# Optimization experiments

Measured on AMD Instinct MI355X. Metric: run time of the kernel, lower is better.

The kernel has to match this reference:

```python
import jax, jax.numpy as jnp
import numpy as np

EPS = 1e-5
GN_GROUPS = 4  # ConvBlock groupnorm num_groups

def _conv3d(x, w, b):
    # x: [B,C,D,H,W], w: [O,I,3,3,3]
    y = jax.lax.conv_general_dilated(x, w, (1, 1, 1), 'SAME',
                                     dimension_numbers=('NCDHW', 'OIDHW', 'NCDHW'))
    return y + b[None, :, None, None, None]

def _groupnorm(x, gamma, beta):
    b, c, d, h, w = x.shape
    xg = x.reshape(b, GN_GROUPS, c // GN_GROUPS, d, h, w)
    m = xg.mean(axis=(2, 3, 4, 5), keepdims=True)
    v = xg.var(axis=(2, 3, 4, 5), keepdims=True)
    xn = ((xg - m) * jax.lax.rsqrt(v + EPS)).reshape(b, c, d, h, w)
    return xn * gamma[None, :, None, None, None] + beta[None, :, None, None, None]

def setup_inputs() -> dict:
    key = jax.random.key(0)
    ks = jax.random.split(key, 8)
    B, C, D, H, W = 4, 64, 16, 16, 16
    R = 4
    f = lambda k, s: jax.random.normal(k, s, dtype=jnp.float32) * 0.05
    return {
        'x': jax.random.normal(ks[0], (B, C, D, H, W), dtype=jnp.float32),
        'w_i': f(ks[1], (C, C, 3, 3, 3)), 'b_i': jnp.zeros((C,), jnp.float32),
        'gamma_i': jnp.ones((C,), jnp.float32), 'beta_i': jnp.zeros((C,), jnp.float32),
        'w_q': f(ks[2], (C // R, C)), 'b_q': jnp.zeros((C // R,), jnp.float32),
        'w_k': f(ks[3], (C // R, C)), 'b_k': jnp.zeros((C // R,), jnp.float32),
        'w_v': f(ks[4], (C, C)), 'b_v': jnp.zeros((C,), jnp.float32),
        'w_o': f(ks[5], (C, C, 3, 3, 3)), 'b_o': jnp.zeros((C,), jnp.float32),
        'gamma_o': jnp.ones((C,), jnp.float32), 'beta_o': jnp.zeros((C,), jnp.float32),
    }

def reference(x, w_i, b_i, gamma_i, beta_i, w_q, b_q, w_k, b_k, w_v, b_v,
              w_o, b_o, gamma_o, beta_o):
    # i_conv: Conv3d(3x3x3) -> GroupNorm(4) -> ReLU
    x = jax.nn.relu(_groupnorm(_conv3d(x, w_i, b_i), gamma_i, beta_i))
    b, c, d, h, w = x.shape
    n = d * h * w
    xf = x.reshape(b, c, n)
    # spatial attention (groups=1): conv1x1 projections as channel matmuls
    q = jnp.einsum('oc,bcn->bon', w_q, xf) + b_q[None, :, None]   # [b, c/r, n]
    k = jnp.einsum('oc,bcn->bon', w_k, xf) + b_k[None, :, None]   # [b, c/r, n]
    v = jnp.einsum('oc,bcn->bon', w_v, xf) + b_v[None, :, None]   # [b, c,   n]
    A = jax.nn.softmax(jnp.einsum('bqn,bqm->bnm', q, k), axis=-1)  # [b, n, n]
    # ans = bmm(value, A^T): ans[b,c,m] = sum_n v[b,c,n] * A[b,m,n]
    sa = jnp.einsum('bcn,bmn->bcm', v, A).reshape(b, c, d, h, w)
    # channel attention
    Ac = jax.nn.softmax(jnp.einsum('bcn,bdn->bcd', xf, xf), axis=-1)  # [b, c, c]
    ca = jnp.einsum('bcd,bdn->bcn', Ac, xf).reshape(b, c, d, h, w)
    y = x + sa + ca
    # o_conv
    return jax.nn.relu(_groupnorm(_conv3d(y, w_o, b_o), gamma_o, beta_o))
```

## Files before the change

kernel.cpp:

```cpp
#include <hip/hip_runtime.h>

#define OFF_X1  0
#define OFF_SA  1048576
#define OFF_QT  2097152
#define OFF_KT  2359296
#define OFF_VB  2621440
#define OFF_YT  3145728
#define OFF_XB  3670016
#define OFF_AC  4194304
#define OFF_WBI 4210688
#define OFF_WBO 4265984
#define OFF_PT  4321280
#define OFF_PO  4325376
#define OFF_MS  6422528
#define WS_NEED ((size_t)6553600 * 4)

typedef __attribute__((ext_vector_type(8))) short short8v;
typedef __attribute__((ext_vector_type(4))) short short4v;
typedef __attribute__((ext_vector_type(4))) float f32x4;

__device__ __forceinline__ ushort f2bf(float f) {
  union { float f; unsigned u; } v; v.f = f;
  unsigned r = (v.u + 0x7fffu + ((v.u >> 16) & 1u)) >> 16;
  return (ushort)r;
}
__device__ __forceinline__ float bf2f(ushort u) {
  union { unsigned u; float f; } v; v.u = ((unsigned)u) << 16;
  return v.f;
}
__device__ __forceinline__ float max3f(float a, float b, float c) {
  return fmaxf(fmaxf(a, b), c);
}

__device__ __forceinline__ void gld_lds16(const ushort* g, ushort* l) {
  __builtin_amdgcn_global_load_lds(
      (const __attribute__((address_space(1))) unsigned*)(unsigned long long)g,
      (__attribute__((address_space(3))) unsigned*)(unsigned long long)l,
      16, 0, 0);
}

__global__ __launch_bounds__(256) void cvt_k(const float* __restrict__ x, ushort* __restrict__ xb,
    float* __restrict__ pt, const float* __restrict__ wi, const float* __restrict__ wo,
    ushort* __restrict__ wbi, ushort* __restrict__ wbo, float* __restrict__ acr) {
  __shared__ ushort tl[64 * 72];
  int blk = blockIdx.x;
  int t = threadIdx.x;
  if (blk < 256) {
    int b = blk >> 6;
    int n0 = (blk & 63) * 64;
    int ci = t >> 2, q = t & 3;
    const float* src = x + (size_t)(b * 64 + ci) * 4096 + n0 + q * 16;
    #pragma unroll
    for (int i = 0; i < 4; ++i) {
      float4 v = *reinterpret_cast<const float4*>(src + i * 4);
      tl[(q * 16 + i * 4 + 0) * 72 + ci] = f2bf(v.x);
      tl[(q * 16 + i * 4 + 1) * 72 + ci] = f2bf(v.y);
      tl[(q * 16 + i * 4 + 2) * 72 + ci] = f2bf(v.z);
      tl[(q * 16 + i * 4 + 3) * 72 + ci] = f2bf(v.w);
    }
    __syncthreads();
    int n = t >> 2, qq = t & 3;
    ushort* dst = xb + (size_t)(b * 4096 + n0 + n) * 64 + qq * 16;
    *reinterpret_cast<short8v*>(dst) = *reinterpret_cast<const short8v*>(&tl[n * 72 + qq * 16]);
    *reinterpret_cast<short8v*>(dst + 8) = *reinterpret_cast<const short8v*>(&tl[n * 72 + qq * 16 + 8]);
  } else if (blk < 1120) {
    int idx = (blk - 256) * 256 + t;
    const float* w = idx < 110592 ? wi : wo;
    ushort* wb = idx < 110592 ? wbi : wbo;
    int j = idx < 110592 ? idx : idx - 110592;
    int ci = j & 63, tap = (j >> 6) % 27, co = j / (64 * 27);
    wb[j] = f2bf(w[(co * 64 + ci) * 27 + tap]);
  } else {
    int idx = (blk - 1120) * 256 + t;
    acr[idx] = 0.f;
    if (blk == 1120 && t < 128) pt[t] = 0.f;
  }
}

__global__ __launch_bounds__(256) void conv_mfma_k(const ushort* __restrict__ xt,
    const ushort* __restrict__ wb, const float* __restrict__ bias, float* __restrict__ out,
    float* __restrict__ ptg, const ushort* __restrict__ zbuf) {
  __shared__ __align__(16) ushort xls[2624 * 8];
  __shared__ float sh_st[16];
  int blk = blockIdx.x;
  int h0 = (blk & 3) * 4;
  int d0 = (blk >> 2) & 15;
  int b  = blk >> 6;
  int tid = threadIdx.x;

  const ushort* xtb = xt + (size_t)b * 4096 * 64;
  {
    int wv0 = tid >> 6, ln = tid & 63;
    #pragma unroll
    for (int it = 0; it < 11; ++it) {
      int clbase = (it * 4 + wv0) * 64;
      if (it == 10) {
        if (wv0 != 0) break;
        clbase = 2560;
      }
      int cl = clbase + ln;
      int c2 = cl & 7;
      int rw = cl >> 3;
      int w_s = rw % 18;
      int rowi = rw / 18;
      int dz = rowi / 6, h_s = rowi - dz * 6;
      int d = d0 + dz - 1, h = h0 + h_s - 1, w = w_s - 1;
      int csrc = c2 ^ (w_s & 7);
      const ushort* g = (d >= 0 && d < 16 && h >= 0 && h < 16 && w >= 0 && w < 16)
          ? xtb + (size_t)(d * 256 + h * 16 + w) * 64 + (csrc << 3)
          : zbuf;
      gld_lds16(g, xls + clbase * 8);
    }
  }
  __syncthreads();

  int wv = tid >> 6, l = tid & 63;
  int wn = wv >> 1, wc = wv & 1;
  int lm = l & 15, lg = l >> 4;

  f32x4 acc[2][2] = {};
  const ushort* wbase0 = wb + (size_t)((wc * 2 + 0) * 16 + lm) * 1728 + lg * 8;
  const ushort* wbase1 = wb + (size_t)((wc * 2 + 1) * 16 + lm) * 1728 + lg * 8;

  #pragma unroll 6
  for (int s = 0; s < 54; ++s) {
    int tap = s >> 1, c0h = s & 1;
    int dz = tap / 9, dyx = tap - dz * 9;
    int dy = dyx / 3, dx = dyx - dy * 3;
    int wrow = lm + dx;
    int chunk = ((c0h * 4 + lg) ^ (wrow & 7)) << 3;
    int r0 = ((dz * 6 + wn * 2 + dy) * 18 + wrow) * 64 + chunk;
    short8v a0 = *reinterpret_cast<const short8v*>(&xls[r0]);
    short8v a1 = *reinterpret_cast<const short8v*>(&xls[r0 + 18 * 64]);
    short8v b0 = *reinterpret_cast<const short8v*>(wbase0 + s * 32);
    short8v b1 = *reinterpret_cast<const short8v*>(wbase1 + s * 32);
    acc[0][0] = __builtin_amdgcn_mfma_f32_16x16x32_bf16(a0, b0, acc[0][0], 0, 0, 0);
    acc[0][1] = __builtin_amdgcn_mfma_f32_16x16x32_bf16(a0, b1, acc[0][1], 0, 0, 0);
    acc[1][0] = __builtin_amdgcn_mfma_f32_16x16x32_bf16(a1, b0, acc[1][0], 0, 0, 0);
    acc[1][1] = __builtin_amdgcn_mfma_f32_16x16x32_bf16(a1, b1, acc[1][1], 0, 0, 0);
  }

  float gs[2], gss[2];
  #pragma unroll
  for (int j = 0; j < 2; ++j) {
    gs[j] = 0.f; gss[j] = 0.f;
    int co = (wc * 2 + j) * 16 + lm;
    float bs = bias[co];
    #pragma unroll
    for (int i = 0; i < 2; ++i) {
      int hh = h0 + wn * 2 + i;
      float4 o;
      o.x = acc[i][j][0] + bs; o.y = acc[i][j][1] + bs;
      o.z = acc[i][j][2] + bs; o.w = acc[i][j][3] + bs;
      gs[j]  += o.x + o.y + o.z + o.w;
      gss[j] = fmaf(o.x, o.x, gss[j]); gss[j] = fmaf(o.y, o.y, gss[j]);
      gss[j] = fmaf(o.z, o.z, gss[j]); gss[j] = fmaf(o.w, o.w, gss[j]);
      *reinterpret_cast<float4*>(&out[(size_t)(b * 64 + co) * 4096 + d0 * 256 + hh * 16 + lg * 4]) = o;
    }
  }
  #pragma unroll
  for (int j = 0; j < 2; ++j) {
    #pragma unroll
    for (int off = 32; off > 0; off >>= 1) {
      gs[j]  += __shfl_xor(gs[j], off);
      gss[j] += __shfl_xor(gss[j], off);
    }
    if (l == 0) { sh_st[wv * 4 + j * 2] = gs[j]; sh_st[wv * 4 + j * 2 + 1] = gss[j]; }
  }
  __syncthreads();
  if (tid < 8) {
    int g = tid >> 1, w2 = tid & 1;
    int wcg = g >> 1, j = g & 1;
    float v = sh_st[wcg * 4 + j * 2 + w2] + sh_st[(wcg + 2) * 4 + j * 2 + w2];
    atomicAdd(&ptg[(b * 4 + g) * 2 + w2], v);
  }
}

__global__ __launch_bounds__(256) void gn_apply_k(const float* __restrict__ t, const float* __restrict__ pt,
    const float* __restrict__ gamma, const float* __restrict__ beta, float* __restrict__ out) {
  int idx4 = blockIdx.x * 256 + threadIdx.x;
  int c = (idx4 >> 10) & 63, b = idx4 >> 16;
  int bg = b * 4 + (c >> 4);
  float s0 = pt[bg * 2], ss0 = pt[bg * 2 + 1];
  float m = s0 * (1.f / 65536.f);
  float r = rsqrtf(ss0 * (1.f / 65536.f) - m * m + 1e-5f);
  float ga = r * gamma[c], bb2 = beta[c] - m * r * gamma[c];
  float4 v = *reinterpret_cast<const float4*>(t + (size_t)idx4 * 4);
  float4 o;
  o.x = fmaxf(fmaf(v.x, ga, bb2), 0.f);
  o.y = fmaxf(fmaf(v.y, ga, bb2), 0.f);
  o.z = fmaxf(fmaf(v.z, ga, bb2), 0.f);
  o.w = fmaxf(fmaf(v.w, ga, bb2), 0.f);
  *reinterpret_cast<float4*>(out + (size_t)idx4 * 4) = o;
}

__global__ __launch_bounds__(256) void projgram_k(const float* __restrict__ t0, const float* __restrict__ pt0,
    const float* __restrict__ gamma, const float* __restrict__ beta,
    const float* __restrict__ wq, const float* __restrict__ bq,
    const float* __restrict__ wk, const float* __restrict__ bk,
    const float* __restrict__ wv_, const float* __restrict__ bv,
    ushort* __restrict__ qt, ushort* __restrict__ kt, ushort* __restrict__ vt,
    float* __restrict__ acr) {
  __shared__ __align__(16) float smem[64 * 68];
  int blk = blockIdx.x;
  int tid = threadIdx.x;
  if (blk < 256) {
    float* xls = smem;
    int b = blk >> 6, n0 = (blk & 63) * 64;
    {
      int ci = tid >> 2, q = tid & 3;
      int bg = b * 4 + (ci >> 4);
      float s0 = pt0[bg * 2], ss0 = pt0[bg * 2 + 1];
      float m = s0 * (1.f / 65536.f);
      float rv = rsqrtf(ss0 * (1.f / 65536.f) - m * m + 1e-5f);
      float ga = rv * gamma[ci], bb2 = beta[ci] - m * rv * gamma[ci];
      const float* src = t0 + (size_t)(b * 64 + ci) * 4096 + n0 + q * 16;
      #pragma unroll
      for (int i = 0; i < 4; ++i) {
        float4 v = *reinterpret_cast<const float4*>(src + i * 4);
        float* d = &xls[ci * 68 + q * 16 + i * 4];
        d[0] = fmaxf(fmaf(v.x, ga, bb2), 0.f);
        d[1] = fmaxf(fmaf(v.y, ga, bb2), 0.f);
        d[2] = fmaxf(fmaf(v.z, ga, bb2), 0.f);
        d[3] = fmaxf(fmaf(v.w, ga, bb2), 0.f);
      }
    }
    __syncthreads();
    int n = tid & 63, og = tid >> 6;
    float xr[64];
    #pragma unroll
    for (int c = 0; c < 64; ++c) xr[c] = xls[c * 68 + n];
    if (og < 2) {
      const float* w  = og == 0 ? wq : wk;
      const float* bb = og == 0 ? bq : bk;
      float scale = og == 0 ? 1.4426950408889634f : 1.0f;
      ushort* outp = og == 0 ? qt : kt;
      union { ushort u[16]; short8v v[2]; } pk;
      #pragma unroll
      for (int o = 0; o < 16; ++o) {
        const float* wr = w + o * 64;
        float acc = bb[o];
        #pragma unroll
        for (int c = 0; c < 64; ++c) acc = fmaf(wr[c], xr[c], acc);
        pk.u[o] = f2bf(acc * scale);
      }
      ushort* dst = outp + (size_t)(b * 4096 + n0 + n) * 32;
      *reinterpret_cast<short8v*>(dst) = pk.v[0];
      *reinterpret_cast<short8v*>(dst + 8) = pk.v[1];
      short8v z = {};
      *reinterpret_cast<short8v*>(dst + 16) = z;
      *reinterpret_cast<short8v*>(dst + 24) = z;
    } else {
      int o0 = (og - 2) * 32;
      #pragma unroll
      for (int o = 0; o < 32; ++o) {
        const float* wr = wv_ + (o0 + o) * 64;
        float acc = bv[o0 + o];
        #pragma unroll
        for (int c = 0; c < 64; ++c) acc = fmaf(wr[c], xr[c], acc);
        vt[(size_t)(b * 64 + o0 + o) * 4096 + n0 + n] = f2bf(acc);
      }
    }
  } else {
    ushort* hi = (ushort*)smem;
    ushort* lo = hi + 4096;
    int gblk = blk - 256;
    int b = gblk >> 5, ks = gblk & 31;
    int wv = tid >> 6, l = tid & 63, lm = l & 15, lg = l >> 4;
    int wr = wv >> 1, wd = wv & 1;
    f32x4 acc[2][2] = {};
    int sr = tid >> 2, sq = tid & 3;
    int bg = b * 4 + (sr >> 4);
    float s0p = pt0[bg * 2], ss0p = pt0[bg * 2 + 1];
    float mq = s0p * (1.f / 65536.f);
    float rq = rsqrtf(ss0p * (1.f / 65536.f) - mq * mq + 1e-5f);
    float ga = rq * gamma[sr], bb2 = beta[sr] - mq * rq * gamma[sr];
    const float* xb = t0 + (size_t)b * 262144;

    for (int kt2 = 0; kt2 < 2; ++kt2) {
      int n0 = ks * 128 + kt2 * 64;
      __syncthreads();
      const float* src = xb + (size_t)sr * 4096 + n0 + sq * 16;
      #pragma unroll
      for (int c2 = 0; c2 < 2; ++c2) {
        int chunk = sq * 2 + c2;
        int dchunk = chunk ^ (sr & 7);
        short8v hvv, lvv;
        #pragma unroll
        for (int j = 0; j < 8; ++j) {
          float v = fmaxf(fmaf(src[c2 * 8 + j], ga, bb2), 0.f);
          ushort hb = f2bf(v);
          union { float f; unsigned u; } uu; uu.u = ((unsigned)hb) << 16;
          hvv[j] = (short)hb;
          lvv[j] = (short)f2bf(v - uu.f);
        }
        *reinterpret_cast<short8v*>(hi + sr * 64 + dchunk * 8) = hvv;
        *reinterpret_cast<short8v*>(lo + sr * 64 + dchunk * 8) = lvv;
      }
      __syncthreads();
      #pragma unroll
      for (int kk = 0; kk < 2; ++kk) {
        short8v ah[2], al[2], bh[2], bl[2];
        #pragma unroll
        for (int i = 0; i < 2; ++i) {
          int rc = wr * 32 + i * 16 + lm;
          int ca = ((kk * 4 + lg) ^ (rc & 7)) * 8;
          ah[i] = *reinterpret_cast<const short8v*>(hi + rc * 64 + ca);
          al[i] = *reinterpret_cast<const short8v*>(lo + rc * 64 + ca);
          int rd = wd * 32 + i * 16 + lm;
          int cb = ((kk * 4 + lg) ^ (rd & 7)) * 8;
          bh[i] = *reinterpret_cast<const short8v*>(hi + rd * 64 + cb);
          bl[i] = *reinterpret_cast<const short8v*>(lo + rd * 64 + cb);
        }
        #pragma unroll
        for (int i = 0; i < 2; ++i)
          #pragma unroll
          for (int j = 0; j < 2; ++j) {
            acc[i][j] = __builtin_amdgcn_mfma_f32_16x16x32_bf16(ah[i], bh[j], acc[i][j], 0, 0, 0);
            acc[i][j] = __builtin_amdgcn_mfma_f32_16x16x32_bf16(ah[i], bl[j], acc[i][j], 0, 0, 0);
            acc[i][j] = __builtin_amdgcn_mfma_f32_16x16x32_bf16(al[i], bh[j], acc[i][j], 0, 0, 0);
          }
      }
    }
    float* acb = acr + (size_t)b * 4096;
    #pragma unroll
    for (int i = 0; i < 2; ++i)
      #pragma unroll
      for (int j = 0; j < 2; ++j)
        #pragma unroll
        for (int r = 0; r < 4; ++r) {
          int c = wr * 32 + i * 16 + lg * 4 + r;
          int d = wd * 32 + j * 16 + lm;
          atomicAdd(&acb[c * 64 + d], acc[i][j][r]);
        }
  }
}

#define KP 40
#define VP 72
template<bool SPLIT>
__global__ __launch_bounds__(256) void flash_mfma_k(const ushort* __restrict__ qt,
    const ushort* __restrict__ kt, const ushort* __restrict__ vb, float* __restrict__ sa,
    ushort* __restrict__ pacc, float* __restrict__ pms) {
  __shared__ __align__(16) ushort kls[2][64 * KP];
  __shared__ __align__(16) ushort vls[2][64 * VP];
  __shared__ __align__(16) ushort pls[64 * VP];
  int s, mt, b;
  if (SPLIT) { s = blockIdx.x & 3; mt = (blockIdx.x >> 2) & 63; b = blockIdx.x >> 8; }
  else       { s = 0; mt = blockIdx.x & 63; b = blockIdx.x >> 6; }
  const int NT = SPLIT ? 16 : 64;
  int m0 = mt * 64;
  int kofs = s * 1024;
  int tid = threadIdx.x;
  int w = tid >> 6, l = tid & 63;
  int lm = l & 15, lg = l >> 4;

  short8v qf = *reinterpret_cast<const short8v*>(
      qt + (size_t)(b * 4096 + m0 + w * 16 + lm) * 32 + lg * 8);

  f32x4 acc[4] = {};
  float M = -1e30f, S = 0.f;

  int sr = tid >> 2, sq = tid & 3;
  const ushort* ksrc = kt + (size_t)b * 4096 * 32 + (size_t)kofs * 32 + (size_t)sr * 32 + sq * 8;
  const ushort* vsrc = vb + (size_t)b * 64 * 4096 + (size_t)sr * 4096 + kofs + sq * 16;
  int koff = sr * KP + sq * 8;
  int voff = sr * VP + sq * 16;

  {
    short8v kr = *reinterpret_cast<const short8v*>(ksrc);
    short8v v0 = *reinterpret_cast<const short8v*>(vsrc);
    short8v v1 = *reinterpret_cast<const short8v*>(vsrc + 8);
    *reinterpret_cast<short8v*>(&kls[0][koff]) = kr;
    *reinterpret_cast<short8v*>(&vls[0][voff]) = v0;
    *reinterpret_cast<short8v*>(&vls[0][voff + 8]) = v1;
  }

  ushort* plb = &pls[(w * 16 + lm) * VP];

  #pragma unroll 2
  for (int it = 0; it < NT; ++it) {
    int cur = it & 1;
    int nx = it < NT - 1 ? it + 1 : NT - 1;
    short8v knr = *reinterpret_cast<const short8v*>(ksrc + (size_t)nx * 2048);
    short8v vn0 = *reinterpret_cast<const short8v*>(vsrc + nx * 64);
    short8v vn1 = *reinterpret_cast<const short8v*>(vsrc + nx * 64 + 8);

    __syncthreads();

    const ushort* kb  = &kls[cur][0];
    const ushort* vbk = &vls[cur][0];

    f32x4 sf[4];
    #pragma unroll
    for (int nt = 0; nt < 4; ++nt) {
      short8v kf = *reinterpret_cast<const short8v*>(&kb[(nt * 16 + lm) * KP + lg * 8]);
      f32x4 z = {};
      sf[nt] = __builtin_amdgcn_mfma_f32_16x16x32_bf16(kf, qf, z, 0, 0, 0);
    }

    float t0_ = max3f(sf[0][0], sf[0][1], sf[0][2]);
    float t1_ = max3f(sf[0][3], sf[1][0], sf[1][1]);
    float t2_ = max3f(sf[1][2], sf[1][3], sf[2][0]);
    float t3_ = max3f(sf[2][1], sf[2][2], sf[2][3]);
    float t4_ = max3f(sf[3][0], sf[3][1], sf[3][2]);
    float tmax = fmaxf(max3f(t0_, t1_, t2_), max3f(t3_, t4_, sf[3][3]));
    tmax = fmaxf(tmax, __shfl_xor(tmax, 16));
    tmax = fmaxf(tmax, __shfl_xor(tmax, 32));
    if (!__all(tmax <= M)) {
      float Mn = fmaxf(M, tmax);
      float sc = __builtin_amdgcn_exp2f(M - Mn);
      M = Mn;
      S *= sc;
      #pragma unroll
      for (int ct = 0; ct < 4; ++ct)
        #pragma unroll
        for (int r = 0; r < 4; ++r) acc[ct][r] *= sc;
    }
    float tsum = 0.f;
    float p[16];
    #pragma unroll
    for (int nt = 0; nt < 4; ++nt)
      #pragma unroll
      for (int r = 0; r < 4; ++r) {
        float e = __builtin_amdgcn_exp2f(sf[nt][r] - M);
        p[nt * 4 + r] = e;
        tsum += e;
      }
    tsum += __shfl_xor(tsum, 16);
    tsum += __shfl_xor(tsum, 32);
    S += tsum;

    #pragma unroll
    for (int nt = 0; nt < 4; ++nt) {
      unsigned p01, p23;
      asm("v_cvt_pk_bf16_f32 %0, %1, %2" : "=v"(p01) : "v"(p[nt * 4 + 0]), "v"(p[nt * 4 + 1]));
      asm("v_cvt_pk_bf16_f32 %0, %1, %2" : "=v"(p23) : "v"(p[nt * 4 + 2]), "v"(p[nt * 4 + 3]));
      union { unsigned u[2]; short4v v; } pk;
      pk.u[0] = p01; pk.u[1] = p23;
      *reinterpret_cast<short4v*>(plb + nt * 16 + lg * 4) = pk.v;
    }
    asm volatile("s_waitcnt lgkmcnt(0)" ::: "memory");
    __builtin_amdgcn_sched_barrier(0);

    #pragma unroll
    for (int nh = 0; nh < 2; ++nh) {
      short8v pf = *reinterpret_cast<const short8v*>(plb + nh * 32 + lg * 8);
      #pragma unroll
      for (int ct = 0; ct < 4; ++ct) {
        short8v vf = *reinterpret_cast<const short8v*>(&vbk[(ct * 16 + lm) * VP + nh * 32 + lg * 8]);
        acc[ct] = __builtin_amdgcn_mfma_f32_16x16x32_bf16(vf, pf, acc[ct], 0, 0, 0);
      }
    }

    if (it < NT - 1) {
      *reinterpret_cast<short8v*>(&kls[cur ^ 1][koff]) = knr;
      *reinterpret_cast<short8v*>(&vls[cur ^ 1][voff]) = vn0;
      *reinterpret_cast<short8v*>(&vls[cur ^ 1][voff + 8]) = vn1;
    }
  }

  if (SPLIT) {
    int blk2 = (b * 64 + mt) * 4 + s;
    ushort* pa = pacc + (size_t)blk2 * 4096;
    #pragma unroll
    for (int ct = 0; ct < 4; ++ct)
      #pragma unroll
      for (int r = 0; r < 4; ++r)
        pa[(ct * 16 + lg * 4 + r) * 64 + w * 16 + lm] = f2bf(acc[ct][r]);
    if (l < 16) {
      pms[(size_t)blk2 * 128 + (w * 16 + lm) * 2]     = M;
      pms[(size_t)blk2 * 128 + (w * 16 + lm) * 2 + 1] = S;
    }
  } else {
    float inv = 1.f / S;
    #pragma unroll
    for (int ct = 0; ct < 4; ++ct)
      #pragma unroll
      for (int r = 0; r < 4; ++r)
        sa[(size_t)(b * 64 + ct * 16 + lg * 4 + r) * 4096 + m0 + w * 16 + lm] = acc[ct][r] * inv;
  }
}

template<int NSPLIT>
__global__ __launch_bounds__(256) void ca_apply_k(const float* __restrict__ t0,
    const float* __restrict__ pt0, const float* __restrict__ gamma, const float* __restrict__ beta,
    const float* __restrict__ acr, const float* __restrict__ sa,
    const ushort* __restrict__ pacc, const float* __restrict__ pms, ushort* __restrict__ yt) {
  __shared__ float x1f[64 * 72];
  __shared__ float acf[64 * 72];
  __shared__ float wls[4 * 64];
  int b = blockIdx.x >> 6, mt = blockIdx.x & 63;
  int n0 = mt * 64;
  int tid = threadIdx.x;
  {
    int d = tid >> 2, q = tid & 3;
    int bg = b * 4 + (d >> 4);
    float s0p = pt0[bg * 2], ss0p = pt0[bg * 2 + 1];
    float mq = s0p * (1.f / 65536.f);
    float rq = rsqrtf(ss0p * (1.f / 65536.f) - mq * mq + 1e-5f);
    float ga = rq * gamma[d], bb2 = beta[d] - mq * rq * gamma[d];
    const float* xs = t0 + (size_t)(b * 64 + d) * 4096 + n0 + q * 16;
    const float* as = acr + (size_t)(b * 64 + d) * 64 + q * 16;
    #pragma unroll
    for (int i = 0; i < 4; ++i) {
      float4 v = *reinterpret_cast<const float4*>(xs + i * 4);
      x1f[d * 72 + q * 16 + i * 4 + 0] = fmaxf(fmaf(v.x, ga, bb2), 0.f);
      x1f[d * 72 + q * 16 + i * 4 + 1] = fmaxf(fmaf(v.y, ga, bb2), 0.f);
      x1f[d * 72 + q * 16 + i * 4 + 2] = fmaxf(fmaf(v.z, ga, bb2), 0.f);
      x1f[d * 72 + q * 16 + i * 4 + 3] = fmaxf(fmaf(v.w, ga, bb2), 0.f);
      float4 a = *reinterpret_cast<const float4*>(as + i * 4);
      acf[d * 72 + q * 16 + i * 4 + 0] = a.x;
      acf[d * 72 + q * 16 + i * 4 + 1] = a.y;
      acf[d * 72 + q * 16 + i * 4 + 2] = a.z;
      acf[d * 72 + q * 16 + i * 4 + 3] = a.w;
    }
  }
  if (NSPLIT > 1 && tid < 64) {
    int m = tid;
    size_t msb = (size_t)(b * 64 + mt) * NSPLIT * 128;
    float Ms[NSPLIT], Ss[NSPLIT];
    float Mg = -1e30f;
    #pragma unroll
    for (int s = 0; s < NSPLIT; ++s) {
      Ms[s] = pms[msb + s * 128 + m * 2];
      Ss[s] = pms[msb + s * 128 + m * 2 + 1];
      Mg = fmaxf(Mg, Ms[s]);
    }
    float Stot = 0.f;
    #pragma unroll
    for (int s = 0; s < NSPLIT; ++s) {
      float wv = __builtin_amdgcn_exp2f(Ms[s] - Mg);
      wls[s * 64 + m] = wv;
      Stot += wv * Ss[s];
    }
    float inv = 1.f / Stot;
    #pragma unroll
    for (int s = 0; s < NSPLIT; ++s) wls[s * 64 + m] *= inv;
  }
  __syncthreads();
  {
    int r = tid >> 2, q4 = tid & 3;
    float* row = &acf[r * 72 + q4 * 16];
    float mx = -1e30f;
    #pragma unroll
    for (int i = 0; i < 16; ++i) mx = fmaxf(mx, row[i]);
    mx = fmaxf(mx, __shfl_xor(mx, 1));
    mx = fmaxf(mx, __shfl_xor(mx, 2));
    float e[16];
    float sum = 0.f;
    #pragma unroll
    for (int i = 0; i < 16; ++i) { e[i] = __expf(row[i] - mx); sum += e[i]; }
    sum += __shfl_xor(sum, 1);
    sum += __shfl_xor(sum, 2);
    float inv = 1.f / sum;
    #pragma unroll
    for (int i = 0; i < 16; ++i) row[i] = e[i] * inv;
  }
  __syncthreads();
  int m = tid & 63, cg = tid >> 6;
  float sval[16];
  if (NSPLIT > 1) {
    #pragma unroll
    for (int ci = 0; ci < 16; ++ci) sval[ci] = 0.f;
    const ushort* pb = pacc + (size_t)(b * 64 + mt) * NSPLIT * 4096;
    #pragma unroll
    for (int s = 0; s < NSPLIT; ++s) {
      float wv = wls[s * 64 + m];
      #pragma unroll
      for (int ci = 0; ci < 16; ++ci)
        sval[ci] = fmaf(wv, bf2f(pb[s * 4096 + (cg * 16 + ci) * 64 + m]), sval[ci]);
    }
  } else {
    #pragma unroll
    for (int ci = 0; ci < 16; ++ci)
      sval[ci] = sa[(size_t)(b * 64 + cg * 16 + ci) * 4096 + n0 + m];
  }
  float xcol[64];
  #pragma unroll
  for (int d = 0; d < 64; ++d) xcol[d] = x1f[d * 72 + m];
  union { ushort u[16]; short8v v[2]; } pk;
  #pragma unroll
  for (int ci = 0; ci < 16; ++ci) {
    int c = cg * 16 + ci;
    float o = xcol[c] + sval[ci];
    const float* ar = &acf[c * 72];
    #pragma unroll
    for (int d4 = 0; d4 < 16; ++d4) {
      float4 a4 = *reinterpret_cast<const float4*>(ar + d4 * 4);
      o = fmaf(a4.x, xcol[d4 * 4 + 0], o);
      o = fmaf(a4.y, xcol[d4 * 4 + 1], o);
      o = fmaf(a4.z, xcol[d4 * 4 + 2], o);
      o = fmaf(a4.w, xcol[d4 * 4 + 3], o);
    }
    pk.u[ci] = f2bf(o);
  }
  ushort* dst = yt + (size_t)(b * 4096 + n0 + m) * 64 + cg * 16;
  *reinterpret_cast<short8v*>(dst) = pk.v[0];
  *reinterpret_cast<short8v*>(dst + 8) = pk.v[1];
}

extern "C" void kernel_launch(void* const* d_in, const int* in_sizes, int n_in,
                              void* d_out, int out_size, void* d_ws, size_t ws_size,
                              hipStream_t stream) {
  const float* x       = (const float*)d_in[0];
  const float* w_i     = (const float*)d_in[1];
  const float* b_i     = (const float*)d_in[2];
  const float* gamma_i = (const float*)d_in[3];
  const float* beta_i  = (const float*)d_in[4];
  const float* w_q     = (const float*)d_in[5];
  const float* b_q     = (const float*)d_in[6];
  const float* w_k     = (const float*)d_in[7];
  const float* b_k     = (const float*)d_in[8];
  const float* w_v     = (const float*)d_in[9];
  const float* b_v     = (const float*)d_in[10];
  const float* w_o     = (const float*)d_in[11];
  const float* b_o     = (const float*)d_in[12];
  const float* gamma_o = (const float*)d_in[13];
  const float* beta_o  = (const float*)d_in[14];
  float* ws = (float*)d_ws;
  float* t0 = ws + OFF_X1;
  ushort* qt  = (ushort*)(ws + OFF_QT);
  ushort* kt  = (ushort*)(ws + OFF_KT);
  ushort* vbp = (ushort*)(ws + OFF_VB);
  float* yb = ws + OFF_SA;
  ushort* ytp = (ushort*)(ws + OFF_YT);
  ushort* xbp = (ushort*)(ws + OFF_XB);
  float* acr = ws + OFF_AC;
  ushort* wbi = (ushort*)(ws + OFF_WBI);
  ushort* wbo = (ushort*)(ws + OFF_WBO);
  float* pt0 = ws + OFF_PT;
  float* pt1 = pt0 + 32;
  const ushort* zbuf = (const ushort*)(pt0 + 96);
  ushort* pacc = (ushort*)(ws + OFF_PO);
  float* pms  = ws + OFF_MS;
  float* outp = (float*)d_out;
  bool split = ws_size >= WS_NEED;

  cvt_k<<<1184, 256, 0, stream>>>(x, xbp, pt0, w_i, w_o, wbi, wbo, acr);

  conv_mfma_k<<<256, 256, 0, stream>>>(xbp, wbi, b_i, t0, pt0, zbuf);

  projgram_k<<<384, 256, 0, stream>>>(t0, pt0, gamma_i, beta_i,
                                      w_q, b_q, w_k, b_k, w_v, b_v, qt, kt, vbp, acr);

  if (split)
    flash_mfma_k<true><<<1024, 256, 0, stream>>>(qt, kt, vbp, yb, pacc, pms);
  else
    flash_mfma_k<false><<<256, 256, 0, stream>>>(qt, kt, vbp, yb, pacc, pms);

  if (split)
    ca_apply_k<4><<<256, 256, 0, stream>>>(t0, pt0, gamma_i, beta_i, acr, yb, pacc, pms, ytp);
  else
    ca_apply_k<1><<<256, 256, 0, stream>>>(t0, pt0, gamma_i, beta_i, acr, yb, pacc, pms, ytp);

  conv_mfma_k<<<256, 256, 0, stream>>>(ytp, wbo, b_o, t0, pt1, zbuf);
  gn_apply_k<<<1024, 256, 0, stream>>>(t0, pt1, gamma_o, beta_o, outp);
}
```

Baseline: 116.3 us.

## Double threads per block in conv and channel-attention kernels, reorder projgram blocks

The 3D conv kernel moves from 4 to 8 waves per block, each wave covering one 16-channel output slice with 2 MFMA accumulators instead of 4. The channel-attention apply kernel also moves to 512 threads, with each thread handling 8 channels instead of 16. In projgram, the gram-matrix blocks are now scheduled first, ahead of the projection blocks. The aim is more latency hiding and more waves per CU on a grid of only 256 blocks, at the cost of redundant A-operand LDS reads across waves and per-thread redundant xcol loads.

After: 114.8 us. Within noise of the previous version (-1.3%).

```diff
diff --git a/kernel.cpp b/kernel.cpp
--- a/kernel.cpp
+++ b/kernel.cpp
@@ -77,7 +77,7 @@
   }
 }
 
-__global__ __launch_bounds__(256) void conv_mfma_k(const ushort* __restrict__ xt,
+__global__ __launch_bounds__(512) void conv_mfma_k(const ushort* __restrict__ xt,
     const ushort* __restrict__ wb, const float* __restrict__ bias, float* __restrict__ out,
     float* __restrict__ ptg, const ushort* __restrict__ zbuf) {
   __shared__ __align__(16) ushort xls[2624 * 8];
@@ -92,12 +92,10 @@
   {
     int wv0 = tid >> 6, ln = tid & 63;
     #pragma unroll
-    for (int it = 0; it < 11; ++it) {
-      int clbase = (it * 4 + wv0) * 64;
-      if (it == 10) {
-        if (wv0 != 0) break;
-        clbase = 2560;
-      }
+    for (int it = 0; it < 6; ++it) {
+      int clbase;
+      if (it < 5) clbase = (it * 8 + wv0) * 64;
+      else { if (wv0 != 0) break; clbase = 2560; }
       int cl = clbase + ln;
       int c2 = cl & 7;
       int rw = cl >> 3;
@@ -115,12 +113,11 @@
   __syncthreads();
 
   int wv = tid >> 6, l = tid & 63;
-  int wn = wv >> 1, wc = wv & 1;
+  int wc4 = wv & 3, wn = wv >> 2;
   int lm = l & 15, lg = l >> 4;
 
-  f32x4 acc[2][2] = {};
-  const ushort* wbase0 = wb + (size_t)((wc * 2 + 0) * 16 + lm) * 1728 + lg * 8;
-  const ushort* wbase1 = wb + (size_t)((wc * 2 + 1) * 16 + lm) * 1728 + lg * 8;
+  f32x4 acc[2] = {};
+  const ushort* wbase = wb + (size_t)((wc4 * 16 + lm) * 1728) + lg * 8;
 
   #pragma unroll 6
   for (int s = 0; s < 54; ++s) {
@@ -132,46 +129,35 @@
     int r0 = ((dz * 6 + wn * 2 + dy) * 18 + wrow) * 64 + chunk;
     short8v a0 = *reinterpret_cast<const short8v*>(&xls[r0]);
     short8v a1 = *reinterpret_cast<const short8v*>(&xls[r0 + 18 * 64]);
-    short8v b0 = *reinterpret_cast<const short8v*>(wbase0 + s * 32);
-    short8v b1 = *reinterpret_cast<const short8v*>(wbase1 + s * 32);
-    acc[0][0] = __builtin_amdgcn_mfma_f32_16x16x32_bf16(a0, b0, acc[0][0], 0, 0, 0);
-    acc[0][1] = __builtin_amdgcn_mfma_f32_16x16x32_bf16(a0, b1, acc[0][1], 0, 0, 0);
-    acc[1][0] = __builtin_amdgcn_mfma_f32_16x16x32_bf16(a1, b0, acc[1][0], 0, 0, 0);
-    acc[1][1] = __builtin_amdgcn_mfma_f32_16x16x32_bf16(a1, b1, acc[1][1], 0, 0, 0);
-  }
-
-  float gs[2], gss[2];
+    short8v b0 = *reinterpret_cast<const short8v*>(wbase + s * 32);
+    acc[0] = __builtin_amdgcn_mfma_f32_16x16x32_bf16(a0, b0, acc[0], 0, 0, 0);
+    acc[1] = __builtin_amdgcn_mfma_f32_16x16x32_bf16(a1, b0, acc[1], 0, 0, 0);
+  }
+
+  float gs = 0.f, gss = 0.f;
+  int co = wc4 * 16 + lm;
+  float bs = bias[co];
   #pragma unroll
-  for (int j = 0; j < 2; ++j) {
-    gs[j] = 0.f; gss[j] = 0.f;
-    int co = (wc * 2 + j) * 16 + lm;
-    float bs = bias[co];
-    #pragma unroll
-    for (int i = 0; i < 2; ++i) {
-      int hh = h0 + wn * 2 + i;
-      float4 o;
-      o.x = acc[i][j][0] + bs; o.y = acc[i][j][1] + bs;
-      o.z = acc[i][j][2] + bs; o.w = acc[i][j][3] + bs;
-      gs[j]  += o.x + o.y + o.z + o.w;
-      gss[j] = fmaf(o.x, o.x, gss[j]); gss[j] = fmaf(o.y, o.y, gss[j]);
-      gss[j] = fmaf(o.z, o.z, gss[j]); gss[j] = fmaf(o.w, o.w, gss[j]);
-      *reinterpret_cast<float4*>(&out[(size_t)(b * 64 + co) * 4096 + d0 * 256 + hh * 16 + lg * 4]) = o;
-    }
+  for (int i = 0; i < 2; ++i) {
+    int hh = h0 + wn * 2 + i;
+    float4 o;
+    o.x = acc[i][0] + bs; o.y = acc[i][1] + bs;
+    o.z = acc[i][2] + bs; o.w = acc[i][3] + bs;
+    gs  += o.x + o.y + o.z + o.w;
+    gss = fmaf(o.x, o.x, gss); gss = fmaf(o.y, o.y, gss);
+    gss = fmaf(o.z, o.z, gss); gss = fmaf(o.w, o.w, gss);
+    *reinterpret_cast<float4*>(&out[(size_t)(b * 64 + co) * 4096 + d0 * 256 + hh * 16 + lg * 4]) = o;
   }
   #pragma unroll
-  for (int j = 0; j < 2; ++j) {
-    #pragma unroll
-    for (int off = 32; off > 0; off >>= 1) {
-      gs[j]  += __shfl_xor(gs[j], off);
-      gss[j] += __shfl_xor(gss[j], off);
-    }
-    if (l == 0) { sh_st[wv * 4 + j * 2] = gs[j]; sh_st[wv * 4 + j * 2 + 1] = gss[j]; }
-  }
+  for (int off = 32; off > 0; off >>= 1) {
+    gs  += __shfl_xor(gs, off);
+    gss += __shfl_xor(gss, off);
+  }
+  if (l == 0) { sh_st[wv * 2] = gs; sh_st[wv * 2 + 1] = gss; }
   __syncthreads();
   if (tid < 8) {
     int g = tid >> 1, w2 = tid & 1;
-    int wcg = g >> 1, j = g & 1;
-    float v = sh_st[wcg * 4 + j * 2 + w2] + sh_st[(wcg + 2) * 4 + j * 2 + w2];
+    float v = sh_st[g * 2 + w2] + sh_st[(4 + g) * 2 + w2];
     atomicAdd(&ptg[(b * 4 + g) * 2 + w2], v);
   }
 }
@@ -204,9 +190,10 @@
   __shared__ __align__(16) float smem[64 * 68];
   int blk = blockIdx.x;
   int tid = threadIdx.x;
-  if (blk < 256) {
+  if (blk >= 128) {
     float* xls = smem;
-    int b = blk >> 6, n0 = (blk & 63) * 64;
+    int pblk = blk - 128;
+    int b = pblk >> 6, n0 = (pblk & 63) * 64;
     {
       int ci = tid >> 2, q = tid & 3;
       int bg = b * 4 + (ci >> 4);
@@ -264,7 +251,7 @@
   } else {
     ushort* hi = (ushort*)smem;
     ushort* lo = hi + 4096;
-    int gblk = blk - 256;
+    int gblk = blk;
     int b = gblk >> 5, ks = gblk & 31;
     int wv = tid >> 6, l = tid & 63, lm = l & 15, lg = l >> 4;
     int wr = wv >> 1, wd = wv & 1;
@@ -483,7 +470,7 @@
 }
 
 template<int NSPLIT>
-__global__ __launch_bounds__(256) void ca_apply_k(const float* __restrict__ t0,
+__global__ __launch_bounds__(512) void ca_apply_k(const float* __restrict__ t0,
     const float* __restrict__ pt0, const float* __restrict__ gamma, const float* __restrict__ beta,
     const float* __restrict__ acr, const float* __restrict__ sa,
     const ushort* __restrict__ pacc, const float* __restrict__ pms, ushort* __restrict__ yt) {
@@ -494,26 +481,26 @@
   int n0 = mt * 64;
   int tid = threadIdx.x;
   {
-    int d = tid >> 2, q = tid & 3;
+    int d = tid >> 3, q = tid & 7;
     int bg = b * 4 + (d >> 4);
     float s0p = pt0[bg * 2], ss0p = pt0[bg * 2 + 1];
     float mq = s0p * (1.f / 65536.f);
     float rq = rsqrtf(ss0p * (1.f / 65536.f) - mq * mq + 1e-5f);
     float ga = rq * gamma[d], bb2 = beta[d] - mq * rq * gamma[d];
-    const float* xs = t0 + (size_t)(b * 64 + d) * 4096 + n0 + q * 16;
-    const float* as = acr + (size_t)(b * 64 + d) * 64 + q * 16;
-    #pragma unroll
-    for (int i = 0; i < 4; ++i) {
+    const float* xs = t0 + (size_t)(b * 64 + d) * 4096 + n0 + q * 8;
+    const float* as = acr + (size_t)(b * 64 + d) * 64 + q * 8;
+    #pragma unroll
+    for (int i = 0; i < 2; ++i) {
       float4 v = *reinterpret_cast<const float4*>(xs + i * 4);
-      x1f[d * 72 + q * 16 + i * 4 + 0] = fmaxf(fmaf(v.x, ga, bb2), 0.f);
-      x1f[d * 72 + q * 16 + i * 4 + 1] = fmaxf(fmaf(v.y, ga, bb2), 0.f);
-      x1f[d * 72 + q * 16 + i * 4 + 2] = fmaxf(fmaf(v.z, ga, bb2), 0.f);
-      x1f[d * 72 + q * 16 + i * 4 + 3] = fmaxf(fmaf(v.w, ga, bb2), 0.f);
+      x1f[d * 72 + q * 8 + i * 4 + 0] = fmaxf(fmaf(v.x, ga, bb2), 0.f);
+      x1f[d * 72 + q * 8 + i * 4 + 1] = fmaxf(fmaf(v.y, ga, bb2), 0.f);
+      x1f[d * 72 + q * 8 + i * 4 + 2] = fmaxf(fmaf(v.z, ga, bb2), 0.f);
+      x1f[d * 72 + q * 8 + i * 4 + 3] = fmaxf(fmaf(v.w, ga, bb2), 0.f);
       float4 a = *reinterpret_cast<const float4*>(as + i * 4);
-      acf[d * 72 + q * 16 + i * 4 + 0] = a.x;
-      acf[d * 72 + q * 16 + i * 4 + 1] = a.y;
-      acf[d * 72 + q * 16 + i * 4 + 2] = a.z;
-      acf[d * 72 + q * 16 + i * 4 + 3] = a.w;
+      acf[d * 72 + q * 8 + i * 4 + 0] = a.x;
+      acf[d * 72 + q * 8 + i * 4 + 1] = a.y;
+      acf[d * 72 + q * 8 + i * 4 + 2] = a.z;
+      acf[d * 72 + q * 8 + i * 4 + 3] = a.w;
     }
   }
   if (NSPLIT > 1 && tid < 64) {
@@ -540,49 +527,51 @@
   }
   __syncthreads();
   {
-    int r = tid >> 2, q4 = tid & 3;
-    float* row = &acf[r * 72 + q4 * 16];
+    int r = tid >> 3, q4 = tid & 7;
+    float* row = &acf[r * 72 + q4 * 8];
     float mx = -1e30f;
     #pragma unroll
-    for (int i = 0; i < 16; ++i) mx = fmaxf(mx, row[i]);
+    for (int i = 0; i < 8; ++i) mx = fmaxf(mx, row[i]);
     mx = fmaxf(mx, __shfl_xor(mx, 1));
     mx = fmaxf(mx, __shfl_xor(mx, 2));
-    float e[16];
+    mx = fmaxf(mx, __shfl_xor(mx, 4));
+    float e[8];
     float sum = 0.f;
     #pragma unroll
-    for (int i = 0; i < 16; ++i) { e[i] = __expf(row[i] - mx); sum += e[i]; }
+    for (int i = 0; i < 8; ++i) { e[i] = __expf(row[i] - mx); sum += e[i]; }
     sum += __shfl_xor(sum, 1);
     sum += __shfl_xor(sum, 2);
+    sum += __shfl_xor(sum, 4);
     float inv = 1.f / sum;
     #pragma unroll
-    for (int i = 0; i < 16; ++i) row[i] = e[i] * inv;
+    for (int i = 0; i < 8; ++i) row[i] = e[i] * inv;
   }
   __syncthreads();
   int m = tid & 63, cg = tid >> 6;
-  float sval[16];
+  float sval[8];
   if (NSPLIT > 1) {
     #pragma unroll
-    for (int ci = 0; ci < 16; ++ci) sval[ci] = 0.f;
+    for (int ci = 0; ci < 8; ++ci) sval[ci] = 0.f;
     const ushort* pb = pacc + (size_t)(b * 64 + mt) * NSPLIT * 4096;
     #pragma unroll
     for (int s = 0; s < NSPLIT; ++s) {
       float wv = wls[s * 64 + m];
       #pragma unroll
-      for (int ci = 0; ci < 16; ++ci)
-        sval[ci] = fmaf(wv, bf2f(pb[s * 4096 + (cg * 16 + ci) * 64 + m]), sval[ci]);
+      for (int ci = 0; ci < 8; ++ci)
+        sval[ci] = fmaf(wv, bf2f(pb[s * 4096 + (cg * 8 + ci) * 64 + m]), sval[ci]);
     }
   } else {
     #pragma unroll
-    for (int ci = 0; ci < 16; ++ci)
-      sval[ci] = sa[(size_t)(b * 64 + cg * 16 + ci) * 4096 + n0 + m];
+    for (int ci = 0; ci < 8; ++ci)
+      sval[ci] = sa[(size_t)(b * 64 + cg * 8 + ci) * 4096 + n0 + m];
   }
   float xcol[64];
   #pragma unroll
   for (int d = 0; d < 64; ++d) xcol[d] = x1f[d * 72 + m];
-  union { ushort u[16]; short8v v[2]; } pk;
+  union { ushort u[8]; short8v v; } pk;
   #pragma unroll
-  for (int ci = 0; ci < 16; ++ci) {
-    int c = cg * 16 + ci;
+  for (int ci = 0; ci < 8; ++ci) {
+    int c = cg * 8 + ci;
     float o = xcol[c] + sval[ci];
     const float* ar = &acf[c * 72];
     #pragma unroll
@@ -595,9 +584,8 @@
     }
     pk.u[ci] = f2bf(o);
   }
-  ushort* dst = yt + (size_t)(b * 4096 + n0 + m) * 64 + cg * 16;
-  *reinterpret_cast<short8v*>(dst) = pk.v[0];
-  *reinterpret_cast<short8v*>(dst + 8) = pk.v[1];
+  ushort* dst = yt + (size_t)(b * 4096 + n0 + m) * 64 + cg * 8;
+  *reinterpret_cast<short8v*>(dst) = pk.v;
 }
 
 extern "C" void kernel_launch(void* const* d_in, const int* in_sizes, int n_in,
@@ -639,7 +627,7 @@
 
   cvt_k<<<1184, 256, 0, stream>>>(x, xbp, pt0, w_i, w_o, wbi, wbo, acr);
 
-  conv_mfma_k<<<256, 256, 0, stream>>>(xbp, wbi, b_i, t0, pt0, zbuf);
+  conv_mfma_k<<<256, 512, 0, stream>>>(xbp, wbi, b_i, t0, pt0, zbuf);
 
   projgram_k<<<384, 256, 0, stream>>>(t0, pt0, gamma_i, beta_i,
                                       w_q, b_q, w_k, b_k, w_v, b_v, qt, kt, vbp, acr);
@@ -650,10 +638,10 @@
     flash_mfma_k<false><<<256, 256, 0, stream>>>(qt, kt, vbp, yb, pacc, pms);
 
   if (split)
-    ca_apply_k<4><<<256, 256, 0, stream>>>(t0, pt0, gamma_i, beta_i, acr, yb, pacc, pms, ytp);
+    ca_apply_k<4><<<256, 512, 0, stream>>>(t0, pt0, gamma_i, beta_i, acr, yb, pacc, pms, ytp);
   else
-    ca_apply_k<1><<<256, 256, 0, stream>>>(t0, pt0, gamma_i, beta_i, acr, yb, pacc, pms, ytp);
-
-  conv_mfma_k<<<256, 256, 0, stream>>>(ytp, wbo, b_o, t0, pt1, zbuf);
+    ca_apply_k<1><<<256, 512, 0, stream>>>(t0, pt0, gamma_i, beta_i, acr, yb, pacc, pms, ytp);
+
+  conv_mfma_k<<<256, 512, 0, stream>>>(ytp, wbo, b_o, t0, pt1, zbuf);
   gn_apply_k<<<1024, 256, 0, stream>>>(t0, pt1, gamma_o, beta_o, outp);
 }
```
